# Kernel optimization log

Hardware: AMD Instinct MI355X
Metric: run time of the kernel (lower is better)

## Reference

```python
import jax, jax.numpy as jnp
import numpy as np

NUM_HEADS = 16
HEAD_SIZE = 64
HIDDEN = NUM_HEADS * HEAD_SIZE  # 1024


def setup_inputs() -> dict:
    key = jax.random.key(0)
    ks = jax.random.split(key, 9)
    B, S1, S2 = 8, 1024, 1024
    scale = 1.0 / np.sqrt(HIDDEN)
    inp = {
        "s1_hidden_states": jax.random.normal(ks[0], (B, S1, HIDDEN), jnp.float32),
        "s2_hidden_states": jax.random.normal(ks[1], (B, S2, HIDDEN), jnp.float32),
        "s2_attention_mask": jnp.zeros((B, 1, 1, S2), jnp.float32),
        "Wq": jax.random.normal(ks[2], (HIDDEN, HIDDEN), jnp.float32) * scale,
        "bq": jnp.zeros((HIDDEN,), jnp.float32),
        "Wk": jax.random.normal(ks[3], (HIDDEN, HIDDEN), jnp.float32) * scale,
        "bk": jnp.zeros((HIDDEN,), jnp.float32),
        "Wv": jax.random.normal(ks[4], (HIDDEN, HIDDEN), jnp.float32) * scale,
        "bv": jnp.zeros((HIDDEN,), jnp.float32),
        "cl_att": 1,
    }
    return inp


def _split_heads(x):
    # [B, S, H*D] -> [B, H, S, D]
    B, S, _ = x.shape
    return x.reshape(B, S, NUM_HEADS, HEAD_SIZE).transpose(0, 2, 1, 3)


def reference(s1_hidden_states, s2_hidden_states, s2_attention_mask,
              Wq, bq, Wk, bk, Wv, bv, cl_att):
    q = _split_heads(s1_hidden_states @ Wq + bq)  # [B,H,S1,D]
    k = _split_heads(s2_hidden_states @ Wk + bk)  # [B,H,S2,D]
    v = _split_heads(s2_hidden_states @ Wv + bv)  # [B,H,S2,D]

    scores = jnp.einsum("bhqd,bhkd->bhqk", q, k) / np.sqrt(HEAD_SIZE)
    scores = scores + s2_attention_mask  # broadcast [B,1,1,S2]
    probs = jax.nn.softmax(scores, axis=-1)
    if cl_att:
        probs = jax.nn.softmax(1.0 - probs + s2_attention_mask, axis=-1)
    # dropout is identity in eval/reference mode
    ctx = jnp.einsum("bhqk,bhkd->bhqd", probs, v)  # [B,H,S1,D]
    B, _, S1, _ = ctx.shape
    return ctx.transpose(0, 2, 1, 3).reshape(B, S1, HIDDEN)
```

## Files before the change

### kernel.cpp

```cpp
#include <hip/hip_runtime.h>
#include <hip/hip_bf16.h>

typedef unsigned short u16;
typedef __attribute__((ext_vector_type(8))) short bf16x8;
typedef __attribute__((ext_vector_type(4))) float f32x4;
typedef __attribute__((ext_vector_type(4))) unsigned u32x4;

#define L2E 1.4426950408889634f

__device__ __forceinline__ u16 f2bf(float f) {
  unsigned u = __float_as_uint(f);
  u = u + 0x7fffu + ((u >> 16) & 1u);
  return (u16)(u >> 16);
}
__device__ __forceinline__ unsigned cvtpk(float a, float b) {
  unsigned r;
  asm("v_cvt_pk_bf16_f32 %0, %1, %2" : "=v"(r) : "v"(a), "v"(b));
  return r;
}
__device__ __forceinline__ float lo16(unsigned v) { return __uint_as_float(v << 16); }
__device__ __forceinline__ float hi16(unsigned v) { return __uint_as_float(v & 0xffff0000u); }

__global__ void wtrans3(const float* __restrict__ Wq, const float* __restrict__ Wk,
                        const float* __restrict__ Wv,
                        u16* __restrict__ Wtq, u16* __restrict__ Wtk, u16* __restrict__ Wtv) {
  int z = blockIdx.z;
  const float* W = (z == 0) ? Wq : (z == 1) ? Wk : Wv;
  u16* Wt = (z == 0) ? Wtq : (z == 1) ? Wtk : Wtv;
  __shared__ float T[32][33];
  int k0 = blockIdx.y * 32, n0 = blockIdx.x * 32;
  int tx = threadIdx.x, ty = threadIdx.y;
  #pragma unroll
  for (int j = 0; j < 4; ++j) T[ty + 8*j][tx] = W[(size_t)(k0 + ty + 8*j) * 1024 + n0 + tx];
  __syncthreads();
  #pragma unroll
  for (int j = 0; j < 4; ++j) Wt[(size_t)(n0 + ty + 8*j) * 1024 + k0 + tx] = f2bf(T[tx][ty + 8*j]);
}

__global__ __launch_bounds__(256) void qkv_gemm3(const float* __restrict__ S1, const float* __restrict__ S2,
                                                 const u16* __restrict__ Wtq, const u16* __restrict__ Wtk,
                                                 const u16* __restrict__ Wtv,
                                                 const float* __restrict__ bq, const float* __restrict__ bk,
                                                 const float* __restrict__ bv,
                                                 u16* __restrict__ Qo, u16* __restrict__ Ko, u16* __restrict__ Vo) {
  int bid = blockIdx.x;
  int xcd = bid & 7, idx = bid >> 3;
  int nblk = idx & 7, pair = idx >> 3;
  int zy = xcd * 24 + pair;
  int z = zy >> 6, y = zy & 63;
  int m0 = y * 128, n0 = nblk * 128;

  const float* Xf  = (z == 0) ? S1 : S2;
  const u16* Wt  = (z == 0) ? Wtq : (z == 1) ? Wtk : Wtv;
  const float* bias = (z == 0) ? bq : (z == 1) ? bk : bv;
  u16* outp = (z == 0) ? Qo : (z == 1) ? Ko : Vo;

  __shared__ __align__(16) u16 As[2][128 * 32];
  __shared__ __align__(16) u16 Bs[2][128 * 32];
  int tid = threadIdx.x;
  int w = tid >> 6, l = tid & 63;
  int wm = w >> 1, wn = w & 1;
  int lq = l & 15, g = l >> 4;
  const int4* Ws = (const int4*)Wt;

  const float4* aSrc[2]; int aDst[2];
  #pragma unroll
  for (int c_ = 0; c_ < 2; ++c_) {
    int i_ = c_ * 256 + tid;
    int row_ = i_ >> 2, kc_ = (i_ & 3) ^ ((row_ >> 1) & 3);
    aSrc[c_] = (const float4*)(Xf + (size_t)(m0 + row_) * 1024 + kc_ * 8);
    aDst[c_] = i_;
  }

#define BSTAGE(bi, kt) do { _Pragma("unroll")                                                \
    for (int c_ = 0; c_ < 2; ++c_) {                                                        \
      int i_ = c_ * 256 + tid;                                                              \
      int row_ = i_ >> 2, kc_ = (i_ & 3) ^ ((row_ >> 1) & 3);                               \
      __builtin_amdgcn_global_load_lds(                                                     \
          (const __attribute__((address_space(1))) void*)&Ws[(size_t)(n0 + row_) * 128 + (kt) * 4 + kc_], \
          (__attribute__((address_space(3))) void*)&((int4*)Bs[bi])[i_], 16, 0, 0);         \
    } } while (0)

#define ALOAD(kt) do { _Pragma("unroll")                                                    \
    for (int c_ = 0; c_ < 2; ++c_) {                                                        \
      xa[c_][0] = aSrc[c_][(kt) * 8];                                                       \
      xa[c_][1] = aSrc[c_][(kt) * 8 + 1];                                                   \
    } } while (0)

#define AWRITE(bi) do { _Pragma("unroll")                                                   \
    for (int c_ = 0; c_ < 2; ++c_) {                                                        \
      u32x4 pk_;                                                                            \
      pk_[0] = cvtpk(xa[c_][0].x, xa[c_][0].y);                                             \
      pk_[1] = cvtpk(xa[c_][0].z, xa[c_][0].w);                                             \
      pk_[2] = cvtpk(xa[c_][1].x, xa[c_][1].y);                                             \
      pk_[3] = cvtpk(xa[c_][1].z, xa[c_][1].w);                                             \
      *(u32x4*)&As[bi][aDst[c_] * 8] = pk_;                                                 \
    } } while (0)

  int aOff[4], bOff[4];
  #pragma unroll
  for (int mc = 0; mc < 4; ++mc) {
    int rowA = wm * 64 + mc * 16 + lq;
    aOff[mc] = rowA * 32 + ((g ^ ((rowA >> 1) & 3)) * 8);
    int rowB = wn * 64 + mc * 16 + lq;
    bOff[mc] = rowB * 32 + ((g ^ ((rowB >> 1) & 3)) * 8);
  }

  f32x4 acc[4][4] = {};
  float4 xa[2][2];
  ALOAD(0);
  BSTAGE(0, 0);
  AWRITE(0);
  __syncthreads();
  int cur = 0;
  for (int kt = 0; kt < 32; ++kt) {
    if (kt < 31) {
      ALOAD(kt + 1);
      BSTAGE(cur ^ 1, kt + 1);
    }
    bf16x8 a[4], bb[4];
    #pragma unroll
    for (int mc = 0; mc < 4; ++mc) a[mc]  = *(const bf16x8*)&As[cur][aOff[mc]];
    #pragma unroll
    for (int nc = 0; nc < 4; ++nc) bb[nc] = *(const bf16x8*)&Bs[cur][bOff[nc]];
    #pragma unroll
    for (int mc = 0; mc < 4; ++mc)
      #pragma unroll
      for (int nc = 0; nc < 4; ++nc)
        acc[mc][nc] = __builtin_amdgcn_mfma_f32_16x16x32_bf16(a[mc], bb[nc], acc[mc][nc], 0, 0, 0);
    if (kt < 31) AWRITE(cur ^ 1);
    __syncthreads();
    cur ^= 1;
  }
#undef BSTAGE
#undef ALOAD
#undef AWRITE
  #pragma unroll
  for (int nc = 0; nc < 4; ++nc) {
    int n = n0 + wn * 64 + nc * 16 + lq;
    float bvv = bias[n];
    int h = n >> 6, d = n & 63;
    #pragma unroll
    for (int mc = 0; mc < 4; ++mc) {
      int srow_base = m0 + wm * 64 + mc * 16 + g * 4;
      if (z == 2) {
        int b = srow_base >> 10, s = srow_base & 1023;
        ushort4 vv;
        vv.x = f2bf(acc[mc][nc][0] + bvv);
        vv.y = f2bf(acc[mc][nc][1] + bvv);
        vv.z = f2bf(acc[mc][nc][2] + bvv);
        vv.w = f2bf(acc[mc][nc][3] + bvv);
        *(ushort4*)&outp[((size_t)((b * 16 + h) * 64 + d)) * 1024 + s] = vv;
      } else {
        #pragma unroll
        for (int r = 0; r < 4; ++r) {
          int sm = srow_base + r;
          int b = sm >> 10, s = sm & 1023;
          outp[((size_t)((b * 16 + h) * 1024 + s)) * 64 + d] = f2bf(acc[mc][nc][r] + bvv);
        }
      }
    }
  }
}

__global__ __launch_bounds__(256, 2) void attn16(const u16* __restrict__ Q, const u16* __restrict__ K,
                                                 const u16* __restrict__ Vt, const float* __restrict__ mask,
                                                 const int* __restrict__ clp, float* __restrict__ out) {
  __shared__ __align__(16) u16 KVl[2][8192];
  __shared__ __align__(16) float maskL2[1024];
  __shared__ float z1p[4][32];
  __shared__ float z2p[4][32];

  int bid = blockIdx.x;
  int xcd = bid & 7, idx = bid >> 3;
  int bh = xcd * 16 + (idx >> 5);
  int qt = idx & 31;
  int b = bh >> 4, h = bh & 15;
  int tid = threadIdx.x;
  int w = tid >> 6, l = tid & 63;
  int lq = l & 15, g = l >> 4;
  int qb = qt * 32;

  const u16* Kb = K + (size_t)bh * 65536;
  const u16* Vb = Vt + (size_t)bh * 65536;
  int cl = clp[0];

  const u16* kS[4]; int kD[4];
  #pragma unroll
  for (int c_ = 0; c_ < 4; ++c_) {
    int i_ = c_ * 256 + tid, row_ = i_ >> 3, ch_ = i_ & 7;
    int f_ = (row_ & 3) | ((((row_ >> 3) ^ (row_ >> 4)) & 1) << 2);
    kS[c_] = Kb + row_ * 64 + (ch_ ^ f_) * 8;
    kD[c_] = i_ * 8;
  }
  const u16* vS[4]; int vD[4];
  #pragma unroll
  for (int c_ = 0; c_ < 4; ++c_) {
    int i_ = c_ * 256 + tid, row_ = i_ >> 4, ch_ = i_ & 15;
    vS[c_] = Vb + row_ * 1024 + (ch_ ^ (row_ & 15)) * 8;
    vD[c_] = i_ * 8;
  }

#define STAGE_K(bi, t) do { _Pragma("unroll")                                                 \
    for (int c_ = 0; c_ < 4; ++c_)                                                           \
      __builtin_amdgcn_global_load_lds(                                                      \
        (const __attribute__((address_space(1))) void*)(kS[c_] + (t) * 8192),                \
        (__attribute__((address_space(3))) void*)&KVl[bi][kD[c_]], 16, 0, 0); } while (0)

#define STAGE_V(bi, t) do { _Pragma("unroll")                                                 \
    for (int c_ = 0; c_ < 4; ++c_)                                                           \
      __builtin_amdgcn_global_load_lds(                                                      \
        (const __attribute__((address_space(1))) void*)(vS[c_] + (t) * 128),                 \
        (__attribute__((address_space(3))) void*)&KVl[bi][vD[c_]], 16, 0, 0); } while (0)

  STAGE_K(0, 0);

  for (int i = tid; i < 1024; i += 256) maskL2[i] = mask[b * 1024 + i] * L2E;

  bf16x8 qf[2][2];
  #pragma unroll
  for (int qg = 0; qg < 2; ++qg) {
    const u16* Qp = Q + ((size_t)bh * 1024 + qb + qg * 16 + lq) * 64 + g * 8;
    qf[qg][0] = *(const bf16x8*)Qp;
    qf[qg][1] = *(const bf16x8*)(Qp + 32);
  }

  int kOff[2][2];
  #pragma unroll
  for (int c = 0; c < 2; ++c) {
    int row128 = w * 32 + ((lq >> 2) << 3) + c * 4 + (lq & 3);
    int F = (row128 & 3) | ((((row128 >> 3) ^ (row128 >> 4)) & 1) << 2);
    kOff[c][0] = row128 * 64 + ((g ^ F) * 8);
    kOff[c][1] = row128 * 64 + (((g + 4) ^ F) * 8);
  }
  int vOff[4];
  #pragma unroll
  for (int dc = 0; dc < 4; ++dc) {
    int row = dc * 16 + lq;
    vOff[dc] = row * 128 + (((w * 4 + g) ^ (row & 15)) * 8);
  }
  int mBase = w * 32 + g * 8;

  __syncthreads();

  const float sl2e = 0.125f * L2E;
  unsigned sp[64];
  float z1[2] = {0.f, 0.f};
  int cur = 0;
  #pragma unroll
  for (int t = 0; t < 8; ++t) {
    if (t < 7) STAGE_K(cur ^ 1, t + 1);
    else       STAGE_V(0, 0);
    #pragma unroll
    for (int c = 0; c < 2; ++c) {
      bf16x8 kf0 = *(const bf16x8*)&KVl[cur][kOff[c][0]];
      bf16x8 kf1 = *(const bf16x8*)&KVl[cur][kOff[c][1]];
      const float4 mk = *(const float4*)&maskL2[t * 128 + mBase + c * 4];
      #pragma unroll
      for (int qg = 0; qg < 2; ++qg) {
        f32x4 tt = {0.f, 0.f, 0.f, 0.f};
        tt = __builtin_amdgcn_mfma_f32_16x16x32_bf16(kf0, qf[qg][0], tt, 0, 0, 0);
        tt = __builtin_amdgcn_mfma_f32_16x16x32_bf16(kf1, qf[qg][1], tt, 0, 0, 0);
        float e0 = __builtin_amdgcn_exp2f(fmaf(tt[0], sl2e, mk.x));
        float e1 = __builtin_amdgcn_exp2f(fmaf(tt[1], sl2e, mk.y));
        float e2 = __builtin_amdgcn_exp2f(fmaf(tt[2], sl2e, mk.z));
        float e3 = __builtin_amdgcn_exp2f(fmaf(tt[3], sl2e, mk.w));
        z1[qg] += (e0 + e1) + (e2 + e3);
        sp[t * 8 + qg * 4 + c * 2 + 0] = cvtpk(e0, e1);
        sp[t * 8 + qg * 4 + c * 2 + 1] = cvtpk(e2, e3);
      }
    }
    __syncthreads();
    cur ^= 1;
  }

  #pragma unroll
  for (int qg = 0; qg < 2; ++qg) {
    z1[qg] += __shfl_xor(z1[qg], 16);
    z1[qg] += __shfl_xor(z1[qg], 32);
  }
  if (l < 16) { z1p[w][l] = z1[0]; z1p[w][16 + l] = z1[1]; }
  __syncthreads();
  float cr[2];
  #pragma unroll
  for (int qg = 0; qg < 2; ++qg) {
    int q = qg * 16 + lq;
    float Z1 = (z1p[0][q] + z1p[1][q]) + (z1p[2][q] + z1p[3][q]);
    cr[qg] = L2E * __builtin_amdgcn_rcpf(Z1);
  }

  f32x4 acc[2][4] = {};
  float z2[2] = {0.f, 0.f};
  #pragma unroll
  for (int t = 0; t < 8; ++t) {
    if (t < 7) STAGE_V((t + 1) & 1, t + 1);
    u32x4 pk[2];
    #pragma unroll
    for (int qg = 0; qg < 2; ++qg) {
      if (cl) {
        #pragma unroll
        for (int j = 0; j < 4; ++j) {
          unsigned e = sp[t * 8 + qg * 4 + j];
          float mkA = maskL2[t * 128 + mBase + 2 * j];
          float mkB = maskL2[t * 128 + mBase + 2 * j + 1];
          float pA = __builtin_amdgcn_exp2f(fmaf(-cr[qg], lo16(e), mkA));
          float pB = __builtin_amdgcn_exp2f(fmaf(-cr[qg], hi16(e), mkB));
          z2[qg] += pA + pB;
          pk[qg][j] = cvtpk(pA, pB);
        }
      } else {
        pk[qg] = *(u32x4*)&sp[t * 8 + qg * 4];
      }
    }
    #pragma unroll
    for (int dc = 0; dc < 4; ++dc) {
      bf16x8 vf = *(const bf16x8*)&KVl[t & 1][vOff[dc]];
      #pragma unroll
      for (int qg = 0; qg < 2; ++qg)
        acc[qg][dc] = __builtin_amdgcn_mfma_f32_16x16x32_bf16(
            __builtin_bit_cast(bf16x8, pk[qg]), vf, acc[qg][dc], 0, 0, 0);
    }
    if (t < 7) __syncthreads();
  }

  #pragma unroll
  for (int qg = 0; qg < 2; ++qg) {
    z2[qg] += __shfl_xor(z2[qg], 16);
    z2[qg] += __shfl_xor(z2[qg], 32);
  }
  if (l < 16) { z2p[w][l] = z2[0]; z2p[w][16 + l] = z2[1]; }
  __syncthreads();
  float* redF = (float*)&KVl[0][0];
  if (w > 0) {
    #pragma unroll
    for (int qg = 0; qg < 2; ++qg)
      #pragma unroll
      for (int dc = 0; dc < 4; ++dc)
        #pragma unroll
        for (int r = 0; r < 4; ++r)
          redF[(w - 1) * 2176 + (qg * 16 + g * 4 + r) * 68 + dc * 16 + lq] = acc[qg][dc][r];
  }
  __syncthreads();
  if (w == 0) {
    #pragma unroll
    for (int qg = 0; qg < 2; ++qg) {
      #pragma unroll
      for (int r = 0; r < 4; ++r) {
        int q = qg * 16 + g * 4 + r;
        float phi;
        if (cl) {
          float Z2 = (z2p[0][q] + z2p[1][q]) + (z2p[2][q] + z2p[3][q]);
          phi = __builtin_amdgcn_rcpf(Z2);
        } else {
          float Z1 = (z1p[0][q] + z1p[1][q]) + (z1p[2][q] + z1p[3][q]);
          phi = __builtin_amdgcn_rcpf(Z1);
        }
        size_t orow = ((size_t)(b * 1024 + qb + q)) * 1024 + h * 64;
        #pragma unroll
        for (int dc = 0; dc < 4; ++dc) {
          int dq = q * 68 + dc * 16 + lq;
          float o = acc[qg][dc][r] + redF[dq] + redF[2176 + dq] + redF[4352 + dq];
          out[orow + dc * 16 + lq] = o * phi;
        }
      }
    }
  }
#undef STAGE_K
#undef STAGE_V
}

extern "C" void kernel_launch(void* const* d_in, const int* in_sizes, int n_in,
                              void* d_out, int out_size, void* d_ws, size_t ws_size,
                              hipStream_t stream) {
  const float* s1   = (const float*)d_in[0];
  const float* s2   = (const float*)d_in[1];
  const float* mask = (const float*)d_in[2];
  const float* Wq   = (const float*)d_in[3];
  const float* bq   = (const float*)d_in[4];
  const float* Wk   = (const float*)d_in[5];
  const float* bk   = (const float*)d_in[6];
  const float* Wv   = (const float*)d_in[7];
  const float* bv   = (const float*)d_in[8];
  const int*   cl   = (const int*)d_in[9];
  float* out = (float*)d_out;

  u16* ws  = (u16*)d_ws;
  const size_t M1 = 1024 * 1024;
  u16* Wtq = ws + 16 * M1;
  u16* Wtk = Wtq + M1;
  u16* Wtv = Wtk + M1;
  u16* Qb  = Wtv + M1;
  u16* Kb  = Qb + 8 * M1;
  u16* Vtb = Kb + 8 * M1;

  wtrans3<<<dim3(32, 32, 3), dim3(32, 8), 0, stream>>>(Wq, Wk, Wv, Wtq, Wtk, Wtv);
  qkv_gemm3<<<1536, 256, 0, stream>>>(s1, s2, Wtq, Wtk, Wtv, bq, bk, bv, Qb, Kb, Vtb);
  attn16<<<4096, 256, 0, stream>>>(Qb, Kb, Vtb, mask, cl, out);
}
```

Before: 173.7 us.

## Double GEMM K-tile to 64 with new LDS swizzle and add MFMA priority hints

The QKV GEMM now stages a 64-wide K slice per iteration instead of 32, which halves the number of loop iterations and barriers. It uses a new XOR swizzle for the 64-element rows so LDS bank conflicts stay low. s_setprio is wrapped around the MFMA blocks in both the GEMM and the attention kernel, so waves issuing matrix ops get scheduling priority over those doing loads or exp work. The cost is double the LDS per GEMM block (64KB) and more registers for the staged A data, which may lower occupancy.

```diff
diff --git a/kernel.cpp b/kernel.cpp
--- a/kernel.cpp
+++ b/kernel.cpp
@@ -55,86 +55,100 @@
   const float* bias = (z == 0) ? bq : (z == 1) ? bk : bv;
   u16* outp = (z == 0) ? Qo : (z == 1) ? Ko : Vo;
 
-  __shared__ __align__(16) u16 As[2][128 * 32];
-  __shared__ __align__(16) u16 Bs[2][128 * 32];
+  __shared__ __align__(16) u16 As[2][8192];
+  __shared__ __align__(16) u16 Bs[2][8192];
   int tid = threadIdx.x;
   int w = tid >> 6, l = tid & 63;
   int wm = w >> 1, wn = w & 1;
   int lq = l & 15, g = l >> 4;
   const int4* Ws = (const int4*)Wt;
 
-  const float4* aSrc[2]; int aDst[2];
-  #pragma unroll
-  for (int c_ = 0; c_ < 2; ++c_) {
+  const float4* aSrc[4]; int aDst[4];
+  const int4* bSrc[4]; int bDst[4];
+  #pragma unroll
+  for (int c_ = 0; c_ < 4; ++c_) {
     int i_ = c_ * 256 + tid;
-    int row_ = i_ >> 2, kc_ = (i_ & 3) ^ ((row_ >> 1) & 3);
-    aSrc[c_] = (const float4*)(Xf + (size_t)(m0 + row_) * 1024 + kc_ * 8);
-    aDst[c_] = i_;
+    int row_ = i_ >> 3, ch_ = i_ & 7;
+    int f_ = (row_ & 3) | ((((row_ >> 3) ^ (row_ >> 4)) & 1) << 2);
+    aSrc[c_] = (const float4*)(Xf + (size_t)(m0 + row_) * 1024) + (ch_ ^ f_) * 2;
+    aDst[c_] = i_ * 8;
+    bSrc[c_] = (const int4*)Ws + (size_t)(n0 + row_) * 128 + (ch_ ^ f_);
+    bDst[c_] = i_;
   }
 
 #define BSTAGE(bi, kt) do { _Pragma("unroll")                                                \
-    for (int c_ = 0; c_ < 2; ++c_) {                                                        \
-      int i_ = c_ * 256 + tid;                                                              \
-      int row_ = i_ >> 2, kc_ = (i_ & 3) ^ ((row_ >> 1) & 3);                               \
+    for (int c_ = 0; c_ < 4; ++c_)                                                          \
       __builtin_amdgcn_global_load_lds(                                                     \
-          (const __attribute__((address_space(1))) void*)&Ws[(size_t)(n0 + row_) * 128 + (kt) * 4 + kc_], \
-          (__attribute__((address_space(3))) void*)&((int4*)Bs[bi])[i_], 16, 0, 0);         \
+          (const __attribute__((address_space(1))) void*)(bSrc[c_] + (kt) * 8),             \
+          (__attribute__((address_space(3))) void*)&((int4*)Bs[bi])[bDst[c_]], 16, 0, 0);   \
+    } while (0)
+
+#define ALOAD(kt) do { _Pragma("unroll")                                                    \
+    for (int c_ = 0; c_ < 4; ++c_) {                                                        \
+      xa[c_][0] = aSrc[c_][(kt) * 16];                                                      \
+      xa[c_][1] = aSrc[c_][(kt) * 16 + 1];                                                  \
     } } while (0)
 
-#define ALOAD(kt) do { _Pragma("unroll")                                                    \
-    for (int c_ = 0; c_ < 2; ++c_) {                                                        \
-      xa[c_][0] = aSrc[c_][(kt) * 8];                                                       \
-      xa[c_][1] = aSrc[c_][(kt) * 8 + 1];                                                   \
-    } } while (0)
-
 #define AWRITE(bi) do { _Pragma("unroll")                                                   \
-    for (int c_ = 0; c_ < 2; ++c_) {                                                        \
+    for (int c_ = 0; c_ < 4; ++c_) {                                                        \
       u32x4 pk_;                                                                            \
       pk_[0] = cvtpk(xa[c_][0].x, xa[c_][0].y);                                             \
       pk_[1] = cvtpk(xa[c_][0].z, xa[c_][0].w);                                             \
       pk_[2] = cvtpk(xa[c_][1].x, xa[c_][1].y);                                             \
       pk_[3] = cvtpk(xa[c_][1].z, xa[c_][1].w);                                             \
-      *(u32x4*)&As[bi][aDst[c_] * 8] = pk_;                                                 \
+      *(u32x4*)&As[bi][aDst[c_]] = pk_;                                                     \
     } } while (0)
 
-  int aOff[4], bOff[4];
+  int aOff[4][2], bOff[4][2];
   #pragma unroll
   for (int mc = 0; mc < 4; ++mc) {
     int rowA = wm * 64 + mc * 16 + lq;
-    aOff[mc] = rowA * 32 + ((g ^ ((rowA >> 1) & 3)) * 8);
+    int FA = (rowA & 3) | ((((rowA >> 3) ^ (rowA >> 4)) & 1) << 2);
+    aOff[mc][0] = rowA * 64 + ((g ^ FA) * 8);
+    aOff[mc][1] = rowA * 64 + (((g + 4) ^ FA) * 8);
     int rowB = wn * 64 + mc * 16 + lq;
-    bOff[mc] = rowB * 32 + ((g ^ ((rowB >> 1) & 3)) * 8);
-  }
+    int FB = (rowB & 3) | ((((rowB >> 3) ^ (rowB >> 4)) & 1) << 2);
+    bOff[mc][0] = rowB * 64 + ((g ^ FB) * 8);
+    bOff[mc][1] = rowB * 64 + (((g + 4) ^ FB) * 8);
+  }
+
+#define MFMA32(bi) do { _Pragma("unroll")                                                   \
+    for (int c_ = 0; c_ < 2; ++c_) {                                                        \
+      bf16x8 a_[4], bb_[4];                                                                 \
+      _Pragma("unroll")                                                                     \
+      for (int mc = 0; mc < 4; ++mc) a_[mc]  = *(const bf16x8*)&As[bi][aOff[mc][c_]];       \
+      _Pragma("unroll")                                                                     \
+      for (int nc = 0; nc < 4; ++nc) bb_[nc] = *(const bf16x8*)&Bs[bi][bOff[nc][c_]];       \
+      __builtin_amdgcn_s_setprio(1);                                                        \
+      _Pragma("unroll")                                                                     \
+      for (int mc = 0; mc < 4; ++mc)                                                        \
+        _Pragma("unroll")                                                                   \
+        for (int nc = 0; nc < 4; ++nc)                                                      \
+          acc[mc][nc] = __builtin_amdgcn_mfma_f32_16x16x32_bf16(a_[mc], bb_[nc], acc[mc][nc], 0, 0, 0); \
+      __builtin_amdgcn_s_setprio(0);                                                        \
+    } } while (0)
 
   f32x4 acc[4][4] = {};
-  float4 xa[2][2];
+  float4 xa[4][2];
   ALOAD(0);
   BSTAGE(0, 0);
   AWRITE(0);
   __syncthreads();
   int cur = 0;
-  for (int kt = 0; kt < 32; ++kt) {
-    if (kt < 31) {
+  for (int kt = 0; kt < 16; ++kt) {
+    if (kt < 15) {
       ALOAD(kt + 1);
       BSTAGE(cur ^ 1, kt + 1);
     }
-    bf16x8 a[4], bb[4];
-    #pragma unroll
-    for (int mc = 0; mc < 4; ++mc) a[mc]  = *(const bf16x8*)&As[cur][aOff[mc]];
-    #pragma unroll
-    for (int nc = 0; nc < 4; ++nc) bb[nc] = *(const bf16x8*)&Bs[cur][bOff[nc]];
-    #pragma unroll
-    for (int mc = 0; mc < 4; ++mc)
-      #pragma unroll
-      for (int nc = 0; nc < 4; ++nc)
-        acc[mc][nc] = __builtin_amdgcn_mfma_f32_16x16x32_bf16(a[mc], bb[nc], acc[mc][nc], 0, 0, 0);
-    if (kt < 31) AWRITE(cur ^ 1);
+    MFMA32(cur);
+    if (kt < 15) AWRITE(cur ^ 1);
     __syncthreads();
     cur ^= 1;
   }
 #undef BSTAGE
 #undef ALOAD
 #undef AWRITE
+#undef MFMA32
   #pragma unroll
   for (int nc = 0; nc < 4; ++nc) {
     int n = n0 + wn * 64 + nc * 16 + lq;
@@ -163,7 +177,7 @@
   }
 }
 
-__global__ __launch_bounds__(256, 2) void attn16(const u16* __restrict__ Q, const u16* __restrict__ K,
+__global__ __launch_bounds__(256, 2) void attn17(const u16* __restrict__ Q, const u16* __restrict__ K,
                                                  const u16* __restrict__ Vt, const float* __restrict__ mask,
                                                  const int* __restrict__ clp, float* __restrict__ out) {
   __shared__ __align__(16) u16 KVl[2][8192];
@@ -259,8 +273,10 @@
       #pragma unroll
       for (int qg = 0; qg < 2; ++qg) {
         f32x4 tt = {0.f, 0.f, 0.f, 0.f};
+        __builtin_amdgcn_s_setprio(1);
         tt = __builtin_amdgcn_mfma_f32_16x16x32_bf16(kf0, qf[qg][0], tt, 0, 0, 0);
         tt = __builtin_amdgcn_mfma_f32_16x16x32_bf16(kf1, qf[qg][1], tt, 0, 0, 0);
+        __builtin_amdgcn_s_setprio(0);
         float e0 = __builtin_amdgcn_exp2f(fmaf(tt[0], sl2e, mk.x));
         float e1 = __builtin_amdgcn_exp2f(fmaf(tt[1], sl2e, mk.y));
         float e2 = __builtin_amdgcn_exp2f(fmaf(tt[2], sl2e, mk.z));
@@ -312,6 +328,7 @@
         pk[qg] = *(u32x4*)&sp[t * 8 + qg * 4];
       }
     }
+    __builtin_amdgcn_s_setprio(1);
     #pragma unroll
     for (int dc = 0; dc < 4; ++dc) {
       bf16x8 vf = *(const bf16x8*)&KVl[t & 1][vOff[dc]];
@@ -320,6 +337,7 @@
         acc[qg][dc] = __builtin_amdgcn_mfma_f32_16x16x32_bf16(
             __builtin_bit_cast(bf16x8, pk[qg]), vf, acc[qg][dc], 0, 0, 0);
     }
+    __builtin_amdgcn_s_setprio(0);
     if (t < 7) __syncthreads();
   }
 
@@ -395,5 +413,5 @@
 
   wtrans3<<<dim3(32, 32, 3), dim3(32, 8), 0, stream>>>(Wq, Wk, Wv, Wtq, Wtk, Wtv);
   qkv_gemm3<<<1536, 256, 0, stream>>>(s1, s2, Wtq, Wtk, Wtv, bq, bk, bv, Qb, Kb, Vtb);
-  attn16<<<4096, 256, 0, stream>>>(Qb, Kb, Vtb, mask, cl, out);
-}
+  attn17<<<4096, 256, 0, stream>>>(Qb, Kb, Vtb, mask, cl, out);
+}
```

After: 176.7 us. About the same (+1.7%).
